# Kernel tuning notes

Measured on AMD Instinct MI355X. Metric: run time of the kernel, lower is better.

Reference implementation:

```python
import jax, jax.numpy as jnp
import numpy as np

C = 256
CK = C // 8  # query/key channels = 32


def setup_inputs() -> dict:
    key = jax.random.key(0)
    ks = jax.random.split(key, 7)
    sc = 0.05
    x = jax.random.normal(ks[0], (4, C, 64, 64), dtype=jnp.float32)
    Wq = jax.random.normal(ks[1], (CK, C), dtype=jnp.float32) * sc
    bq = jax.random.normal(ks[2], (CK,), dtype=jnp.float32) * sc
    Wk = jax.random.normal(ks[3], (CK, C), dtype=jnp.float32) * sc
    bk = jax.random.normal(ks[4], (CK,), dtype=jnp.float32) * sc
    Wv = jax.random.normal(ks[5], (C, C), dtype=jnp.float32) * sc
    bv = jax.random.normal(ks[6], (C,), dtype=jnp.float32) * sc
    gamma = jnp.array([0.5], dtype=jnp.float32)  # nonzero so output/grads are nontrivial
    return {"x": x, "Wq": Wq, "bq": bq, "Wk": Wk, "bk": bk, "Wv": Wv, "bv": bv, "gamma": gamma}


def reference(x, Wq, bq, Wk, bk, Wv, bv, gamma):
    B, Cc, H, W = x.shape
    xf = x.reshape(B, Cc, H * W)  # [B, C, N]
    # 1x1 conv1d == channel-wise matmul
    f = jnp.einsum('kc,bcn->bkn', Wq, xf) + bq[None, :, None]  # [B, CK, N]
    g = jnp.einsum('kc,bcn->bkn', Wk, xf) + bk[None, :, None]  # [B, CK, N]
    h = jnp.einsum('oc,bcn->bon', Wv, xf) + bv[None, :, None]  # [B, C, N]
    # unscaled attention scores: s[b,i,j] = sum_k f[b,k,i] g[b,k,j]
    s = jnp.einsum('bki,bkj->bij', f, g)  # [B, N, N]
    beta = jax.nn.softmax(s, axis=1)      # softmax over query-side axis i (dim=1)
    o = jnp.einsum('bci,bij->bcj', h, beta)  # [B, C, N]
    o = gamma[0] * o
    return o.reshape(B, Cc, H, W)
```

## Files before the change

kernel.cpp:

```cpp
#include <hip/hip_runtime.h>
#include <math.h>

#define BB 4
#define CC 256
#define CKK 32
#define NN 4096
#define TI 32
#define NT (NN / TI)
#define NP (NT / 2)
#define SM_OFF 40.0f

typedef __attribute__((ext_vector_type(8))) short short8v;
typedef __attribute__((ext_vector_type(4))) short short4v;
typedef __attribute__((ext_vector_type(4))) float f32x4;

static __device__ inline unsigned short f2bf(float x) {
    union { float f; unsigned u; } v; v.f = x;
    unsigned r = v.u + 0x7fffu + ((v.u >> 16) & 1u);
    return (unsigned short)(r >> 16);
}
static __device__ inline float bf2f(unsigned short h) {
    union { unsigned u; float f; } v; v.u = ((unsigned)h) << 16;
    return v.f;
}

__global__ __launch_bounds__(256) void prep_w(
    const float* __restrict__ Wq, const float* __restrict__ Wk,
    const float* __restrict__ Wv, unsigned short* __restrict__ Wbf)
{
    int o = blockIdx.x * 256 + threadIdx.x;
    int rb   = o >> 12;
    int rem  = o & 4095;
    int k    = rem >> 9;
    int lane = (rem >> 3) & 63;
    int e    = rem & 7;
    int row  = rb * 16 + (lane & 15);
    int c    = k * 32 + (lane >> 4) * 8 + e;
    float v;
    if (row < 32)      v = Wq[row * 256 + c];
    else if (row < 64) v = Wk[(row - 32) * 256 + c];
    else               v = Wv[(row - 64) * 256 + c];
    Wbf[o] = f2bf(v);
}

__global__ __launch_bounds__(256, 4) void proj_kernel(
    const float* __restrict__ x,
    const unsigned short* __restrict__ Wbf,
    const float* __restrict__ bq, const float* __restrict__ bk,
    const float* __restrict__ bv,
    unsigned short* __restrict__ fF, unsigned short* __restrict__ gT,
    unsigned short* __restrict__ hF)
{
    __shared__ unsigned short xsh[32 * 264];
    __shared__ unsigned short xsl[32 * 264];

    const int t = threadIdx.x;
    const int b = blockIdx.x >> 7;
    const int n_b = (blockIdx.x & 127) * 32;
    const int lane = t & 63;
    const int wave = t >> 6;
    const int jl = lane & 15;
    const int quad = lane >> 4;

    {
        const int q = t & 7, cb = t >> 3;
        #pragma unroll
        for (int cc = 0; cc < 8; ++cc) {
            int c = cb + cc * 32;
            float4 v = *(const float4*)(x + ((size_t)b * CC + c) * NN + n_b + q * 4);
            float vv[4] = {v.x, v.y, v.z, v.w};
            #pragma unroll
            for (int e = 0; e < 4; ++e) {
                int n = q * 4 + e;
                unsigned short h = f2bf(vv[e]);
                unsigned short l = f2bf(vv[e] - bf2f(h));
                xsh[n * 264 + c] = h;
                xsl[n * 264 + c] = l;
            }
        }
    }
    __syncthreads();

    const int rowbase_w = wave * 80;
    #pragma unroll 1
    for (int nt = 0; nt < 2; ++nt) {
        short8v bhi[8], blo[8];
        #pragma unroll
        for (int k = 0; k < 8; ++k) {
            bhi[k] = *(const short8v*)&xsh[(nt * 16 + jl) * 264 + k * 32 + quad * 8];
            blo[k] = *(const short8v*)&xsl[(nt * 16 + jl) * 264 + k * 32 + quad * 8];
        }
        const int ng = n_b + nt * 16 + jl;
        const int it  = ng >> 5;
        const int il  = ng & 31;
        const int ihh = (ng >> 4) & 1;
        #pragma unroll 1
        for (int mt = 0; mt < 5; ++mt) {
            int rowbase = rowbase_w + mt * 16;
            const int rb = rowbase >> 4;
            const unsigned short* wf = Wbf + (size_t)rb * 8 * 512;
            f32x4 acch = (f32x4){0.f, 0.f, 0.f, 0.f};
            f32x4 accl = (f32x4){0.f, 0.f, 0.f, 0.f};
            #pragma unroll
            for (int k = 0; k < 8; ++k) {
                short8v a = *(const short8v*)(wf + (size_t)k * 512 + lane * 8);
                acch = __builtin_amdgcn_mfma_f32_16x16x32_bf16(a, bhi[k], acch, 0, 0, 0);
                accl = __builtin_amdgcn_mfma_f32_16x16x32_bf16(a, blo[k], accl, 0, 0, 0);
            }
            f32x4 acc;
            #pragma unroll
            for (int r = 0; r < 4; ++r) acc[r] = acch[r] + accl[r];
            int rlo = rowbase + quad * 4;
            if (rowbase < 32) {
                float4 bias = *(const float4*)(bq + rlo);
                short4v o;
                o[0] = (short)f2bf(acc[0] + bias.x); o[1] = (short)f2bf(acc[1] + bias.y);
                o[2] = (short)f2bf(acc[2] + bias.z); o[3] = (short)f2bf(acc[3] + bias.w);
                size_t dst = (((size_t)b * NT + it) * 2 + ihh) * 512
                           + (size_t)((rlo >> 3) * 16 + (ng & 15)) * 8 + (rlo & 7);
                *(short4v*)(fF + dst) = o;
            } else if (rowbase < 64) {
                float4 bias = *(const float4*)(bk + rlo - 32);
                short4v o;
                o[0] = (short)f2bf(acc[0] + bias.x); o[1] = (short)f2bf(acc[1] + bias.y);
                o[2] = (short)f2bf(acc[2] + bias.z); o[3] = (short)f2bf(acc[3] + bias.w);
                *(short4v*)(gT + ((size_t)b * NN + ng) * CKK + (rlo - 32)) = o;
            } else {
                const float* bp = bv + rlo - 64;
                #pragma unroll
                for (int r = 0; r < 4; ++r) {
                    int c = rlo - 64 + r;
                    size_t dst = (((size_t)b * NT + it) * 16 + (c >> 4)) * 512
                               + (size_t)((il >> 3) * 16 + (c & 15)) * 8 + (il & 7);
                    hF[dst] = f2bf(acc[r] + bp[r]);
                }
            }
        }
    }
}

__global__ __launch_bounds__(1024, 4) void attn_kernel(
    const unsigned short* __restrict__ fF,
    const unsigned short* __restrict__ gT,
    const unsigned short* __restrict__ hF,
    const float* __restrict__ gamma,
    float* __restrict__ out)
{
    __shared__ unsigned short pa[2][2][4][512];
    __shared__ unsigned short fsh[2][4][512];
    __shared__ float ls[16][16];
    __shared__ float ls2[4][16];

    const int t = threadIdx.x;
    const int lane = t & 63;
    const int wave = t >> 6;
    const int bi = blockIdx.x;
    const int b  = bi & 3;
    const int j0 = (bi >> 2) * 64;
    const int jl = lane & 15;
    const int quad = lane >> 4;
    const int jcq  = wave & 3;
    const int ihq  = (wave >> 2) & 1;
    const int subq = wave >> 3;
    const int cg   = wave;
    const int fsid = subq * 2 + ihq;

    const unsigned short* fFb = fF + (size_t)b * NT * 2 * 512;
    const unsigned short* hFb = hF + (size_t)b * NT * 16 * 512;

    short8v bg = *(const short8v*)(gT + ((size_t)b * NN + j0 + jcq * 16 + jl) * CKK + quad * 8);

    f32x4 acc[4];
    #pragma unroll
    for (int q = 0; q < 4; ++q) acc[q] = (f32x4){0.f, 0.f, 0.f, 0.f};
    float l_run = 0.f;

    const f32x4 zoff = (f32x4){-SM_OFF, -SM_OFF, -SM_OFF, -SM_OFF};

    const int Lw = ((ihq * 2 + (quad >> 1)) * 16 + jl) * 8 + (quad & 1) * 4;

    short8v af0 = *(const short8v*)(fFb + ((size_t)subq * 2 + ihq) * 512 + lane * 8);
    short8v ah0 = *(const short8v*)(hFb + ((size_t)0 * 16 + cg) * 512 + lane * 8);
    short8v ah1 = *(const short8v*)(hFb + ((size_t)1 * 16 + cg) * 512 + lane * 8);
    short8v an0 = *(const short8v*)(hFb + ((size_t)2 * 16 + cg) * 512 + lane * 8);
    short8v an1 = *(const short8v*)(hFb + ((size_t)3 * 16 + cg) * 512 + lane * 8);
    short8v fs0;
    if (wave < 4)
        fs0 = *(const short8v*)(fFb + ((size_t)(2 + (wave >> 1)) * 2 + (wave & 1)) * 512 + lane * 8);
    f32x4 s0 = __builtin_amdgcn_mfma_f32_16x16x32_bf16(af0, bg, zoff, 0, 0, 0);
    {
        float e0 = __expf(s0[0]), e1 = __expf(s0[1]);
        float e2 = __expf(s0[2]), e3 = __expf(s0[3]);
        l_run += (e0 + e1) + (e2 + e3);
        unsigned p01, p23;
        asm("v_cvt_pk_bf16_f32 %0, %1, %2" : "=v"(p01) : "v"(e0), "v"(e1));
        asm("v_cvt_pk_bf16_f32 %0, %1, %2" : "=v"(p23) : "v"(e2), "v"(e3));
        uint2 pw; pw.x = p01; pw.y = p23;
        *(uint2*)&pa[0][subq][jcq][Lw] = pw;
    }
    if (wave < 4)
        *(short8v*)&fsh[1][wave][lane * 8] = fs0;
    asm volatile("s_waitcnt lgkmcnt(0)" ::: "memory");
    __builtin_amdgcn_s_barrier();
    asm volatile("" ::: "memory");

    #pragma unroll 1
    for (int p = 0; p < NP - 1; ++p) {
        const int buf = p & 1;

        short8v af = *(const short8v*)&fsh[buf ^ 1][fsid][lane * 8];
        f32x4 s = __builtin_amdgcn_mfma_f32_16x16x32_bf16(af, bg, zoff, 0, 0, 0);

        short8v fs2;
        if (wave < 4) {
            const int tp2 = (p + 2 < NP ? p + 2 : NP - 1);
            fs2 = *(const short8v*)(fFb + ((size_t)(2 * tp2 + (wave >> 1)) * 2 + (wave & 1)) * 512 + lane * 8);
        }

        const int pq = (p + 2 < NP ? p + 2 : NP - 1);
        short8v aq0 = *(const short8v*)(hFb + ((size_t)(2 * pq) * 16 + cg) * 512 + lane * 8);
        short8v aq1 = *(const short8v*)(hFb + ((size_t)(2 * pq + 1) * 16 + cg) * 512 + lane * 8);

        __builtin_amdgcn_s_setprio(1);
        #pragma unroll
        for (int jc2 = 0; jc2 < 4; ++jc2) {
            short8v bpA = *(const short8v*)&pa[buf][0][jc2][lane * 8];
            acc[jc2] = __builtin_amdgcn_mfma_f32_16x16x32_bf16(ah0, bpA, acc[jc2], 0, 0, 0);
            short8v bpB = *(const short8v*)&pa[buf][1][jc2][lane * 8];
            acc[jc2] = __builtin_amdgcn_mfma_f32_16x16x32_bf16(ah1, bpB, acc[jc2], 0, 0, 0);
        }
        __builtin_amdgcn_s_setprio(0);

        {
            float e0 = __expf(s[0]), e1 = __expf(s[1]);
            float e2 = __expf(s[2]), e3 = __expf(s[3]);
            l_run += (e0 + e1) + (e2 + e3);
            unsigned p01, p23;
            asm("v_cvt_pk_bf16_f32 %0, %1, %2" : "=v"(p01) : "v"(e0), "v"(e1));
            asm("v_cvt_pk_bf16_f32 %0, %1, %2" : "=v"(p23) : "v"(e2), "v"(e3));
            uint2 pw; pw.x = p01; pw.y = p23;
            *(uint2*)&pa[buf ^ 1][subq][jcq][Lw] = pw;
        }
        if (wave < 4)
            *(short8v*)&fsh[buf][wave][lane * 8] = fs2;

        asm volatile("s_waitcnt lgkmcnt(0)" ::: "memory");
        __builtin_amdgcn_s_barrier();
        asm volatile("" ::: "memory");

        ah0 = an0; ah1 = an1; an0 = aq0; an1 = aq1;
    }

    {
        const int buf = (NP - 1) & 1;
        #pragma unroll
        for (int jc2 = 0; jc2 < 4; ++jc2) {
            short8v bpA = *(const short8v*)&pa[buf][0][jc2][lane * 8];
            acc[jc2] = __builtin_amdgcn_mfma_f32_16x16x32_bf16(ah0, bpA, acc[jc2], 0, 0, 0);
            short8v bpB = *(const short8v*)&pa[buf][1][jc2][lane * 8];
            acc[jc2] = __builtin_amdgcn_mfma_f32_16x16x32_bf16(ah1, bpB, acc[jc2], 0, 0, 0);
        }
    }

    l_run += __shfl_xor(l_run, 16, 64);
    l_run += __shfl_xor(l_run, 32, 64);
    if (quad == 0) ls[wave][jl] = l_run;
    __syncthreads();
    if (wave < 4 && quad == 0)
        ls2[wave][jl] = gamma[0] / (((ls[wave][jl] + ls[wave + 4][jl])
                                   + (ls[wave + 8][jl] + ls[wave + 12][jl])));
    __syncthreads();

    #pragma unroll
    for (int jc2 = 0; jc2 < 4; ++jc2) {
        float sc = ls2[jc2][jl];
        f32x4 a = acc[jc2];
        size_t addr = ((size_t)b * CC + cg * 16 + quad * 4) * NN + j0 + jc2 * 16 + jl;
        #pragma unroll
        for (int r = 0; r < 4; ++r)
            out[addr + (size_t)r * NN] = a[r] * sc;
    }
}

extern "C" void kernel_launch(void* const* d_in, const int* in_sizes, int n_in,
                              void* d_out, int out_size, void* d_ws, size_t ws_size,
                              hipStream_t stream) {
    const float* x     = (const float*)d_in[0];
    const float* Wq    = (const float*)d_in[1];
    const float* bq    = (const float*)d_in[2];
    const float* Wk    = (const float*)d_in[3];
    const float* bk    = (const float*)d_in[4];
    const float* Wv    = (const float*)d_in[5];
    const float* bv    = (const float*)d_in[6];
    const float* gamma = (const float*)d_in[7];
    float* out = (float*)d_out;

    unsigned short* Wbf = (unsigned short*)d_ws;
    unsigned short* fF  = Wbf + 320 * 256;
    unsigned short* gT  = fF + (size_t)BB * NN * CKK;
    unsigned short* hF  = gT + (size_t)BB * NN * CKK;

    prep_w<<<320, 256, 0, stream>>>(Wq, Wk, Wv, Wbf);
    proj_kernel<<<BB * (NN / 32), 256, 0, stream>>>(x, Wbf, bq, bk, bv, fF, gT, hF);
    attn_kernel<<<BB * (NN / 64), 1024, 0, stream>>>(fF, gT, hF, gamma, out);
}
```

Before: 142.6 us.

## Split attention block into producer score waves and consumer PV waves

Warp-specializes the 16-wave block so that waves 0-7 compute scores, exponentials and bf16 probabilities into shared memory, while waves 8-15 only run the P·V MFMA accumulation, each covering two channel groups. Before, every wave interleaved score computation with accumulation, and f was staged through shared memory. The aim is to overlap softmax/exp VALU work with matrix work on separate waves and to reuse each probability fragment across two h fragments. In exchange the consumer waves hold twice as many accumulators and prefetch registers, which raises register pressure. Both wave groups must also keep their barrier counts matched.

```diff
diff --git a/kernel.cpp b/kernel.cpp
--- a/kernel.cpp
+++ b/kernel.cpp
@@ -147,8 +147,7 @@
     float* __restrict__ out)
 {
     __shared__ unsigned short pa[2][2][4][512];
-    __shared__ unsigned short fsh[2][4][512];
-    __shared__ float ls[16][16];
+    __shared__ float ls[8][2][16];
     __shared__ float ls2[4][16];
 
     const int t = threadIdx.x;
@@ -159,126 +158,153 @@
     const int j0 = (bi >> 2) * 64;
     const int jl = lane & 15;
     const int quad = lane >> 4;
-    const int jcq  = wave & 3;
-    const int ihq  = (wave >> 2) & 1;
-    const int subq = wave >> 3;
-    const int cg   = wave;
-    const int fsid = subq * 2 + ihq;
 
     const unsigned short* fFb = fF + (size_t)b * NT * 2 * 512;
     const unsigned short* hFb = hF + (size_t)b * NT * 16 * 512;
 
-    short8v bg = *(const short8v*)(gT + ((size_t)b * NN + j0 + jcq * 16 + jl) * CKK + quad * 8);
-
-    f32x4 acc[4];
-    #pragma unroll
-    for (int q = 0; q < 4; ++q) acc[q] = (f32x4){0.f, 0.f, 0.f, 0.f};
-    float l_run = 0.f;
-
     const f32x4 zoff = (f32x4){-SM_OFF, -SM_OFF, -SM_OFF, -SM_OFF};
 
-    const int Lw = ((ihq * 2 + (quad >> 1)) * 16 + jl) * 8 + (quad & 1) * 4;
-
-    short8v af0 = *(const short8v*)(fFb + ((size_t)subq * 2 + ihq) * 512 + lane * 8);
-    short8v ah0 = *(const short8v*)(hFb + ((size_t)0 * 16 + cg) * 512 + lane * 8);
-    short8v ah1 = *(const short8v*)(hFb + ((size_t)1 * 16 + cg) * 512 + lane * 8);
-    short8v an0 = *(const short8v*)(hFb + ((size_t)2 * 16 + cg) * 512 + lane * 8);
-    short8v an1 = *(const short8v*)(hFb + ((size_t)3 * 16 + cg) * 512 + lane * 8);
-    short8v fs0;
-    if (wave < 4)
-        fs0 = *(const short8v*)(fFb + ((size_t)(2 + (wave >> 1)) * 2 + (wave & 1)) * 512 + lane * 8);
-    f32x4 s0 = __builtin_amdgcn_mfma_f32_16x16x32_bf16(af0, bg, zoff, 0, 0, 0);
-    {
-        float e0 = __expf(s0[0]), e1 = __expf(s0[1]);
-        float e2 = __expf(s0[2]), e3 = __expf(s0[3]);
-        l_run += (e0 + e1) + (e2 + e3);
-        unsigned p01, p23;
-        asm("v_cvt_pk_bf16_f32 %0, %1, %2" : "=v"(p01) : "v"(e0), "v"(e1));
-        asm("v_cvt_pk_bf16_f32 %0, %1, %2" : "=v"(p23) : "v"(e2), "v"(e3));
-        uint2 pw; pw.x = p01; pw.y = p23;
-        *(uint2*)&pa[0][subq][jcq][Lw] = pw;
-    }
-    if (wave < 4)
-        *(short8v*)&fsh[1][wave][lane * 8] = fs0;
-    asm volatile("s_waitcnt lgkmcnt(0)" ::: "memory");
-    __builtin_amdgcn_s_barrier();
-    asm volatile("" ::: "memory");
-
-    #pragma unroll 1
-    for (int p = 0; p < NP - 1; ++p) {
-        const int buf = p & 1;
-
-        short8v af = *(const short8v*)&fsh[buf ^ 1][fsid][lane * 8];
-        f32x4 s = __builtin_amdgcn_mfma_f32_16x16x32_bf16(af, bg, zoff, 0, 0, 0);
-
-        short8v fs2;
-        if (wave < 4) {
-            const int tp2 = (p + 2 < NP ? p + 2 : NP - 1);
-            fs2 = *(const short8v*)(fFb + ((size_t)(2 * tp2 + (wave >> 1)) * 2 + (wave & 1)) * 512 + lane * 8);
-        }
-
-        const int pq = (p + 2 < NP ? p + 2 : NP - 1);
-        short8v aq0 = *(const short8v*)(hFb + ((size_t)(2 * pq) * 16 + cg) * 512 + lane * 8);
-        short8v aq1 = *(const short8v*)(hFb + ((size_t)(2 * pq + 1) * 16 + cg) * 512 + lane * 8);
-
-        __builtin_amdgcn_s_setprio(1);
-        #pragma unroll
-        for (int jc2 = 0; jc2 < 4; ++jc2) {
-            short8v bpA = *(const short8v*)&pa[buf][0][jc2][lane * 8];
-            acc[jc2] = __builtin_amdgcn_mfma_f32_16x16x32_bf16(ah0, bpA, acc[jc2], 0, 0, 0);
-            short8v bpB = *(const short8v*)&pa[buf][1][jc2][lane * 8];
-            acc[jc2] = __builtin_amdgcn_mfma_f32_16x16x32_bf16(ah1, bpB, acc[jc2], 0, 0, 0);
-        }
-        __builtin_amdgcn_s_setprio(0);
-
+    if (wave < 8) {
+        const int sub = wave >> 2;
+        const int ihp = (wave >> 1) & 1;
+        const int jcp = wave & 1;
+        const int Lw = ((ihp * 2 + (quad >> 1)) * 16 + jl) * 8 + (quad & 1) * 4;
+
+        short8v bg0 = *(const short8v*)(gT + ((size_t)b * NN + j0 + (2 * jcp) * 16 + jl) * CKK + quad * 8);
+        short8v bg1 = *(const short8v*)(gT + ((size_t)b * NN + j0 + (2 * jcp + 1) * 16 + jl) * CKK + quad * 8);
+
+        float l0 = 0.f, l1 = 0.f;
+
+        short8v af = *(const short8v*)(fFb + ((size_t)sub * 2 + ihp) * 512 + lane * 8);
+        short8v afn = *(const short8v*)(fFb + ((size_t)(2 + sub) * 2 + ihp) * 512 + lane * 8);
         {
-            float e0 = __expf(s[0]), e1 = __expf(s[1]);
-            float e2 = __expf(s[2]), e3 = __expf(s[3]);
-            l_run += (e0 + e1) + (e2 + e3);
-            unsigned p01, p23;
+            f32x4 s0 = __builtin_amdgcn_mfma_f32_16x16x32_bf16(af, bg0, zoff, 0, 0, 0);
+            f32x4 s1 = __builtin_amdgcn_mfma_f32_16x16x32_bf16(af, bg1, zoff, 0, 0, 0);
+            float e0 = __expf(s0[0]), e1 = __expf(s0[1]), e2 = __expf(s0[2]), e3 = __expf(s0[3]);
+            float f0 = __expf(s1[0]), f1 = __expf(s1[1]), f2 = __expf(s1[2]), f3 = __expf(s1[3]);
+            l0 += (e0 + e1) + (e2 + e3);
+            l1 += (f0 + f1) + (f2 + f3);
+            unsigned p01, p23, q01, q23;
             asm("v_cvt_pk_bf16_f32 %0, %1, %2" : "=v"(p01) : "v"(e0), "v"(e1));
             asm("v_cvt_pk_bf16_f32 %0, %1, %2" : "=v"(p23) : "v"(e2), "v"(e3));
+            asm("v_cvt_pk_bf16_f32 %0, %1, %2" : "=v"(q01) : "v"(f0), "v"(f1));
+            asm("v_cvt_pk_bf16_f32 %0, %1, %2" : "=v"(q23) : "v"(f2), "v"(f3));
             uint2 pw; pw.x = p01; pw.y = p23;
-            *(uint2*)&pa[buf ^ 1][subq][jcq][Lw] = pw;
-        }
-        if (wave < 4)
-            *(short8v*)&fsh[buf][wave][lane * 8] = fs2;
-
+            uint2 qw; qw.x = q01; qw.y = q23;
+            *(uint2*)&pa[0][sub][2 * jcp][Lw] = pw;
+            *(uint2*)&pa[0][sub][2 * jcp + 1][Lw] = qw;
+        }
         asm volatile("s_waitcnt lgkmcnt(0)" ::: "memory");
         __builtin_amdgcn_s_barrier();
         asm volatile("" ::: "memory");
 
-        ah0 = an0; ah1 = an1; an0 = aq0; an1 = aq1;
-    }
-
-    {
-        const int buf = (NP - 1) & 1;
+        #pragma unroll 1
+        for (int p = 0; p < NP; ++p) {
+            const int buf = p & 1;
+            if (p + 1 < NP) {
+                f32x4 s0 = __builtin_amdgcn_mfma_f32_16x16x32_bf16(afn, bg0, zoff, 0, 0, 0);
+                f32x4 s1 = __builtin_amdgcn_mfma_f32_16x16x32_bf16(afn, bg1, zoff, 0, 0, 0);
+                {
+                    const int p2 = (p + 2 < NP ? p + 2 : NP - 1);
+                    afn = *(const short8v*)(fFb + ((size_t)(2 * p2 + sub) * 2 + ihp) * 512 + lane * 8);
+                }
+                float e0 = __expf(s0[0]), e1 = __expf(s0[1]), e2 = __expf(s0[2]), e3 = __expf(s0[3]);
+                float f0 = __expf(s1[0]), f1 = __expf(s1[1]), f2 = __expf(s1[2]), f3 = __expf(s1[3]);
+                l0 += (e0 + e1) + (e2 + e3);
+                l1 += (f0 + f1) + (f2 + f3);
+                unsigned p01, p23, q01, q23;
+                asm("v_cvt_pk_bf16_f32 %0, %1, %2" : "=v"(p01) : "v"(e0), "v"(e1));
+                asm("v_cvt_pk_bf16_f32 %0, %1, %2" : "=v"(p23) : "v"(e2), "v"(e3));
+                asm("v_cvt_pk_bf16_f32 %0, %1, %2" : "=v"(q01) : "v"(f0), "v"(f1));
+                asm("v_cvt_pk_bf16_f32 %0, %1, %2" : "=v"(q23) : "v"(f2), "v"(f3));
+                uint2 pw; pw.x = p01; pw.y = p23;
+                uint2 qw; qw.x = q01; qw.y = q23;
+                *(uint2*)&pa[buf ^ 1][sub][2 * jcp][Lw] = pw;
+                *(uint2*)&pa[buf ^ 1][sub][2 * jcp + 1][Lw] = qw;
+            }
+            asm volatile("s_waitcnt lgkmcnt(0)" ::: "memory");
+            __builtin_amdgcn_s_barrier();
+            asm volatile("" ::: "memory");
+        }
+
+        l0 += __shfl_xor(l0, 16, 64);
+        l0 += __shfl_xor(l0, 32, 64);
+        l1 += __shfl_xor(l1, 16, 64);
+        l1 += __shfl_xor(l1, 32, 64);
+        if (quad == 0) { ls[wave][0][jl] = l0; ls[wave][1][jl] = l1; }
+        __syncthreads();
+        if (wave < 4 && quad == 0) {
+            const int jc = wave;
+            const int jp = jc >> 1, sl = jc & 1;
+            ls2[jc][jl] = gamma[0] / (((ls[jp][sl][jl] + ls[jp + 2][sl][jl])
+                                     + (ls[jp + 4][sl][jl] + ls[jp + 6][sl][jl])));
+        }
+        __syncthreads();
+    } else {
+        const int cw = wave - 8;
+        const int cg0 = cw * 2;
+
+        f32x4 acc[8];
+        #pragma unroll
+        for (int q = 0; q < 8; ++q) acc[q] = (f32x4){0.f, 0.f, 0.f, 0.f};
+
+        short8v ahA0 = *(const short8v*)(hFb + ((size_t)0 * 16 + cg0 + 0) * 512 + lane * 8);
+        short8v ahA1 = *(const short8v*)(hFb + ((size_t)0 * 16 + cg0 + 1) * 512 + lane * 8);
+        short8v ahB0 = *(const short8v*)(hFb + ((size_t)1 * 16 + cg0 + 0) * 512 + lane * 8);
+        short8v ahB1 = *(const short8v*)(hFb + ((size_t)1 * 16 + cg0 + 1) * 512 + lane * 8);
+        short8v anA0 = *(const short8v*)(hFb + ((size_t)2 * 16 + cg0 + 0) * 512 + lane * 8);
+        short8v anA1 = *(const short8v*)(hFb + ((size_t)2 * 16 + cg0 + 1) * 512 + lane * 8);
+        short8v anB0 = *(const short8v*)(hFb + ((size_t)3 * 16 + cg0 + 0) * 512 + lane * 8);
+        short8v anB1 = *(const short8v*)(hFb + ((size_t)3 * 16 + cg0 + 1) * 512 + lane * 8);
+        asm volatile("s_waitcnt lgkmcnt(0)" ::: "memory");
+        __builtin_amdgcn_s_barrier();
+        asm volatile("" ::: "memory");
+
+        #pragma unroll 1
+        for (int p = 0; p < NP; ++p) {
+            const int buf = p & 1;
+
+            const int pq = (p + 2 < NP ? p + 2 : NP - 1);
+            short8v aqA0 = *(const short8v*)(hFb + ((size_t)(2 * pq) * 16 + cg0 + 0) * 512 + lane * 8);
+            short8v aqA1 = *(const short8v*)(hFb + ((size_t)(2 * pq) * 16 + cg0 + 1) * 512 + lane * 8);
+            short8v aqB0 = *(const short8v*)(hFb + ((size_t)(2 * pq + 1) * 16 + cg0 + 0) * 512 + lane * 8);
+            short8v aqB1 = *(const short8v*)(hFb + ((size_t)(2 * pq + 1) * 16 + cg0 + 1) * 512 + lane * 8);
+
+            __builtin_amdgcn_s_setprio(1);
+            #pragma unroll
+            for (int jc2 = 0; jc2 < 4; ++jc2) {
+                short8v bpA = *(const short8v*)&pa[buf][0][jc2][lane * 8];
+                acc[jc2 * 2 + 0] = __builtin_amdgcn_mfma_f32_16x16x32_bf16(ahA0, bpA, acc[jc2 * 2 + 0], 0, 0, 0);
+                acc[jc2 * 2 + 1] = __builtin_amdgcn_mfma_f32_16x16x32_bf16(ahA1, bpA, acc[jc2 * 2 + 1], 0, 0, 0);
+                short8v bpB = *(const short8v*)&pa[buf][1][jc2][lane * 8];
+                acc[jc2 * 2 + 0] = __builtin_amdgcn_mfma_f32_16x16x32_bf16(ahB0, bpB, acc[jc2 * 2 + 0], 0, 0, 0);
+                acc[jc2 * 2 + 1] = __builtin_amdgcn_mfma_f32_16x16x32_bf16(ahB1, bpB, acc[jc2 * 2 + 1], 0, 0, 0);
+            }
+            __builtin_amdgcn_s_setprio(0);
+
+            asm volatile("s_waitcnt lgkmcnt(0)" ::: "memory");
+            __builtin_amdgcn_s_barrier();
+            asm volatile("" ::: "memory");
+
+            ahA0 = anA0; ahA1 = anA1; ahB0 = anB0; ahB1 = anB1;
+            anA0 = aqA0; anA1 = aqA1; anB0 = aqB0; anB1 = aqB1;
+        }
+
+        __syncthreads();
+        __syncthreads();
+
         #pragma unroll
         for (int jc2 = 0; jc2 < 4; ++jc2) {
-            short8v bpA = *(const short8v*)&pa[buf][0][jc2][lane * 8];
-            acc[jc2] = __builtin_amdgcn_mfma_f32_16x16x32_bf16(ah0, bpA, acc[jc2], 0, 0, 0);
-            short8v bpB = *(const short8v*)&pa[buf][1][jc2][lane * 8];
-            acc[jc2] = __builtin_amdgcn_mfma_f32_16x16x32_bf16(ah1, bpB, acc[jc2], 0, 0, 0);
-        }
-    }
-
-    l_run += __shfl_xor(l_run, 16, 64);
-    l_run += __shfl_xor(l_run, 32, 64);
-    if (quad == 0) ls[wave][jl] = l_run;
-    __syncthreads();
-    if (wave < 4 && quad == 0)
-        ls2[wave][jl] = gamma[0] / (((ls[wave][jl] + ls[wave + 4][jl])
-                                   + (ls[wave + 8][jl] + ls[wave + 12][jl])));
-    __syncthreads();
-
-    #pragma unroll
-    for (int jc2 = 0; jc2 < 4; ++jc2) {
-        float sc = ls2[jc2][jl];
-        f32x4 a = acc[jc2];
-        size_t addr = ((size_t)b * CC + cg * 16 + quad * 4) * NN + j0 + jc2 * 16 + jl;
-        #pragma unroll
-        for (int r = 0; r < 4; ++r)
-            out[addr + (size_t)r * NN] = a[r] * sc;
+            float sc = ls2[jc2][jl];
+            #pragma unroll
+            for (int cc = 0; cc < 2; ++cc) {
+                f32x4 a = acc[jc2 * 2 + cc];
+                size_t addr = ((size_t)b * CC + cw * 32 + cc * 16 + quad * 4) * NN + j0 + jc2 * 16 + jl;
+                #pragma unroll
+                for (int r = 0; r < 4; ++r)
+                    out[addr + (size_t)r * NN] = a[r] * sc;
+            }
+        }
     }
 }
 
```

New measurement: 139.9 us. No clear change (-1.9%).
